# Performance work log

Hardware: AMD Instinct MI355X
Metric: run time of the kernel (lower is better)

## Reference

```python
import jax, jax.numpy as jnp
import numpy as np

TEMPERATURE = 0.5
EPSILON = 1e-9


def _l2_normalize(x, eps=1e-12):
    # matches torch F.normalize(p=2, dim=-1): x / max(||x||, eps)
    n = jnp.linalg.norm(x, axis=-1, keepdims=True)
    return x / jnp.maximum(n, eps)


def setup_inputs() -> dict:
    key = jax.random.key(0)
    k1, k2, k3 = jax.random.split(key, 3)
    N, D, V = 8192, 128, 3
    H_consensus = jax.random.normal(k1, (N, D), dtype=jnp.float32)
    S_similarity = jax.random.uniform(k2, (N, N), dtype=jnp.float32)
    H_views = jax.random.normal(k3, (V, N, D), dtype=jnp.float32)
    return {"H_consensus": H_consensus, "S_similarity": S_similarity, "H_views": H_views}


def reference(H_consensus, S_similarity, H_views):
    N = H_consensus.shape[0]
    V = H_views.shape[0]
    Hc = _l2_normalize(H_consensus)            # [N, D]
    Hv = _l2_normalize(H_views)                # [V, N, D]
    sim = jnp.einsum('nd,vmd->vnm', Hc, Hv)    # [V, N, N]
    positive = jnp.diagonal(sim, axis1=1, axis2=2) / TEMPERATURE  # [V, N]
    weights = 1.0 - S_similarity               # [N, N], broadcast over V
    denom = jnp.sum(weights * jnp.exp(sim / TEMPERATURE), axis=-1)  # [V, N]
    denom = jnp.maximum(denom, EPSILON)
    loss = -(positive - jnp.log(denom))        # [V, N]
    return jnp.sum(loss) / (N * V)
```

## Files before the change

### kernel.cpp

```cpp
#include <hip/hip_runtime.h>
#include <hip/hip_bf16.h>

constexpr int kN = 8192;
constexpr int kD = 128;
constexpr int kV = 3;
constexpr int kNV = kV * kN;
constexpr int kNChunk = 512;
constexpr int kNTile = 32;
constexpr int kIters = kNChunk / kNTile;
constexpr int kAccStride = 529;

typedef __attribute__((ext_vector_type(8))) short bf16x8;
typedef __attribute__((ext_vector_type(4))) float floatx4;

__device__ __forceinline__ unsigned pack_bf16(float a, float b) {
    unsigned ua = __float_as_uint(a);
    unsigned ub = __float_as_uint(b);
    ua = (ua + 0x7FFFu + ((ua >> 16) & 1u)) >> 16;
    ub = (ub + 0x7FFFu + ((ub >> 16) & 1u)) >> 16;
    return ua | (ub << 16);
}

__global__ void k_normalize(const float* __restrict__ Hc, const float* __restrict__ Hv,
                            unsigned* __restrict__ HcB, unsigned* __restrict__ HvB) {
    int row  = (blockIdx.x * blockDim.x + threadIdx.x) >> 6;
    int lane = threadIdx.x & 63;
    const float* src;
    unsigned* dst;
    float extra;
    if (row < kN) { src = Hc + (size_t)row * kD; dst = HcB + (size_t)row * (kD / 2); extra = 2.0f; }
    else {
        int r = row - kN;
        src = Hv + (size_t)r * kD; dst = HvB + (size_t)r * (kD / 2); extra = 1.0f;
    }
    float2 x = ((const float2*)src)[lane];
    float ss = x.x * x.x + x.y * x.y;
    ss += __shfl_xor(ss, 1);  ss += __shfl_xor(ss, 2);  ss += __shfl_xor(ss, 4);
    ss += __shfl_xor(ss, 8);  ss += __shfl_xor(ss, 16); ss += __shfl_xor(ss, 32);
    float inv = extra * rsqrtf(fmaxf(ss, 1e-24f));
    dst[lane] = pack_bf16(x.x * inv, x.y * inv);
}

__global__ void k_positive(const unsigned* __restrict__ HcB, const unsigned* __restrict__ HvB,
                           float* __restrict__ pos_partial) {
    int row  = (blockIdx.x * blockDim.x + threadIdx.x) >> 6;
    int lane = threadIdx.x & 63;
    int w    = threadIdx.x >> 6;
    int n    = row & (kN - 1);
    unsigned a = HcB[(size_t)n * (kD / 2) + lane];
    unsigned b = HvB[(size_t)row * (kD / 2) + lane];
    float dot = __uint_as_float(a << 16) * __uint_as_float(b << 16)
              + __uint_as_float(a & 0xFFFF0000u) * __uint_as_float(b & 0xFFFF0000u);
    dot += __shfl_xor(dot, 1);  dot += __shfl_xor(dot, 2);  dot += __shfl_xor(dot, 4);
    dot += __shfl_xor(dot, 8);  dot += __shfl_xor(dot, 16); dot += __shfl_xor(dot, 32);
    __shared__ float acc4[4];
    if (lane == 0) acc4[w] = dot;
    __syncthreads();
    if (threadIdx.x == 0)
        atomicAdd(&pos_partial[blockIdx.x & 255], acc4[0] + acc4[1] + acc4[2] + acc4[3]);
}

__launch_bounds__(256, 3)
__global__ void k_main(const unsigned* __restrict__ HcB, const unsigned* __restrict__ HvB,
                       const float* __restrict__ S, float* __restrict__ denom) {
    __shared__ float Stile[2][kNTile * 68];
    __shared__ short Htile[2][kNTile * 136];
    __shared__ float accum[kV * kAccStride];

    const int tid  = threadIdx.x;
    const int w    = tid >> 6;
    const int lane = tid & 63;
    const int col  = lane & 15;
    const int quad = lane >> 4;
    const int m0b  = blockIdx.x * 64;
    const int m0w  = m0b + w * 16;
    const int nbase = blockIdx.y * kNChunk;
    const int sr = tid >> 4;
    const int sc = tid & 15;

    for (int i = tid; i < kV * kAccStride; i += 256) accum[i] = 0.f;

    bf16x8 afrag[kV][4];
#pragma unroll
    for (int v = 0; v < kV; ++v) {
        const short* rowp = (const short*)HvB + ((size_t)(v * kN + m0w + col)) * kD;
#pragma unroll
        for (int kk = 0; kk < 4; ++kk)
            afrag[v][kk] = *(const bf16x8*)(rowp + kk * 32 + quad * 8);
    }

    const short* hc = (const short*)HcB;

    {
        int n0 = nbase;
        float4 sa = *(const float4*)(S + (size_t)(n0 + sr) * kN + m0b + sc * 4);
        float4 sb = *(const float4*)(S + (size_t)(n0 + sr + 16) * kN + m0b + sc * 4);
        float4 ha = *(const float4*)(hc + (size_t)(n0 + sr) * kD + sc * 8);
        float4 hb = *(const float4*)(hc + (size_t)(n0 + sr + 16) * kD + sc * 8);
        *(float4*)&Stile[0][sr * 68 + sc * 4]        = sa;
        *(float4*)&Stile[0][(sr + 16) * 68 + sc * 4] = sb;
        *(float4*)&Htile[0][sr * 136 + sc * 8]        = ha;
        *(float4*)&Htile[0][(sr + 16) * 136 + sc * 8] = hb;
    }
    __syncthreads();

    for (int it = 0; it < kIters; ++it) {
        int itn = (it + 1 < kIters) ? it + 1 : it;
        int n0n = nbase + itn * kNTile;
        float4 sa = *(const float4*)(S + (size_t)(n0n + sr) * kN + m0b + sc * 4);
        float4 sb = *(const float4*)(S + (size_t)(n0n + sr + 16) * kN + m0b + sc * 4);
        float4 ha = *(const float4*)(hc + (size_t)(n0n + sr) * kD + sc * 8);
        float4 hb = *(const float4*)(hc + (size_t)(n0n + sr + 16) * kD + sc * 8);

        const int cur = it & 1;
#pragma unroll
        for (int sub = 0; sub < 2; ++sub) {
            const int nrow = sub * 16 + col;
            bf16x8 bfrag[4];
#pragma unroll
            for (int kk = 0; kk < 4; ++kk)
                bfrag[kk] = *(const bf16x8*)&Htile[cur][nrow * 136 + kk * 32 + quad * 8];
            float4 s4 = *(const float4*)&Stile[cur][nrow * 68 + w * 16 + quad * 4];

            floatx4 acc0 = {0.f,0.f,0.f,0.f}, acc1 = {0.f,0.f,0.f,0.f}, acc2 = {0.f,0.f,0.f,0.f};
#pragma unroll
            for (int kk = 0; kk < 4; ++kk) {
                acc0 = __builtin_amdgcn_mfma_f32_16x16x32_bf16(afrag[0][kk], bfrag[kk], acc0, 0, 0, 0);
                acc1 = __builtin_amdgcn_mfma_f32_16x16x32_bf16(afrag[1][kk], bfrag[kk], acc1, 0, 0, 0);
                acc2 = __builtin_amdgcn_mfma_f32_16x16x32_bf16(afrag[2][kk], bfrag[kk], acc2, 0, 0, 0);
            }
            float w0 = 1.f - s4.x, w1 = 1.f - s4.y, w2 = 1.f - s4.z, w3 = 1.f - s4.w;
            float p0 = w0 * __expf(acc0[0]) + w1 * __expf(acc0[1]) + w2 * __expf(acc0[2]) + w3 * __expf(acc0[3]);
            float p1 = w0 * __expf(acc1[0]) + w1 * __expf(acc1[1]) + w2 * __expf(acc1[2]) + w3 * __expf(acc1[3]);
            float p2 = w0 * __expf(acc2[0]) + w1 * __expf(acc2[1]) + w2 * __expf(acc2[2]) + w3 * __expf(acc2[3]);
            p0 += __shfl_xor(p0, 16); p0 += __shfl_xor(p0, 32);
            p1 += __shfl_xor(p1, 16); p1 += __shfl_xor(p1, 32);
            p2 += __shfl_xor(p2, 16); p2 += __shfl_xor(p2, 32);
            float val = (quad == 0) ? p0 : ((quad == 1) ? p1 : p2);
            if (quad < 3)
                atomicAdd(&accum[quad * kAccStride + it * kNTile + sub * 16 + col], val);
        }

        const int nxt = cur ^ 1;
        *(float4*)&Stile[nxt][sr * 68 + sc * 4]        = sa;
        *(float4*)&Stile[nxt][(sr + 16) * 68 + sc * 4] = sb;
        *(float4*)&Htile[nxt][sr * 136 + sc * 8]        = ha;
        *(float4*)&Htile[nxt][(sr + 16) * 136 + sc * 8] = hb;
        __syncthreads();
    }

    for (int i = tid; i < kV * kNChunk; i += 256) {
        int v = i >> 9, c = i & (kNChunk - 1);
        atomicAdd(&denom[(size_t)v * kN + nbase + c], accum[v * kAccStride + c]);
    }
}

__global__ void k_final(const float* __restrict__ denom, const float* __restrict__ pos_partial,
                        float* __restrict__ out) {
    int idx  = blockIdx.x * 256 + threadIdx.x;
    int lane = threadIdx.x & 63;
    int w    = threadIdx.x >> 6;
    float val = logf(fmaxf(denom[idx], 1e-9f));
    if (blockIdx.x == 0) val -= pos_partial[threadIdx.x];
    val += __shfl_xor(val, 1);  val += __shfl_xor(val, 2);  val += __shfl_xor(val, 4);
    val += __shfl_xor(val, 8);  val += __shfl_xor(val, 16); val += __shfl_xor(val, 32);
    __shared__ float acc4[4];
    if (lane == 0) acc4[w] = val;
    __syncthreads();
    if (threadIdx.x == 0)
        atomicAdd(out, (acc4[0] + acc4[1] + acc4[2] + acc4[3]) * (1.0f / kNV));
}

extern "C" void kernel_launch(void* const* d_in, const int* in_sizes, int n_in,
                              void* d_out, int out_size, void* d_ws, size_t ws_size,
                              hipStream_t stream) {
    const float* Hc = (const float*)d_in[0];
    const float* S  = (const float*)d_in[1];
    const float* Hv = (const float*)d_in[2];

    unsigned* HcB  = (unsigned*)d_ws;
    unsigned* HvB  = HcB + (size_t)kN * (kD / 2);
    float*    den  = (float*)(HvB + (size_t)kV * kN * (kD / 2));
    float*    posp = den + kNV;
    float*    outF = (float*)d_out;

    hipMemsetAsync(den, 0, ((size_t)kNV + 256) * sizeof(float), stream);
    hipMemsetAsync(outF, 0, sizeof(float), stream);

    k_normalize<<<dim3((kN + kV * kN) / 4), 256, 0, stream>>>(Hc, Hv, HcB, HvB);
    k_positive<<<dim3(kNV / 4), 256, 0, stream>>>(HcB, HvB, posp);
    k_main<<<dim3(kN / 64, kN / kNChunk), dim3(256), 0, stream>>>(HcB, HvB, S, den);
    k_final<<<dim3(kNV / 256), dim3(256), 0, stream>>>(den, posp, outF);
}
```

Measured before the change: 431.3 us.

## Load S directly into registers, use exp2 with prescaled Hc, permlane quad reductions

Removes the shared-memory staging of the S tile: each lane now loads its own S values straight from global memory into registers and prefetches the next iteration's values. The Hc normalization scale is folded to 2/ln2 so the hardware exp2 can replace __expf, and the positive term is multiplied by ln2 in the final kernel to compensate. The cross-quad shuffles are replaced with v_permlane16/32_swap inline asm. Per-lane S loads are less coalesced than the old tiled loads, and the inline asm depends on the target supporting these permlane instructions.

```diff
diff --git a/kernel.cpp b/kernel.cpp
--- a/kernel.cpp
+++ b/kernel.cpp
@@ -9,9 +9,17 @@
 constexpr int kNTile = 32;
 constexpr int kIters = kNChunk / kNTile;
 constexpr int kAccStride = 529;
+constexpr float kLn2 = 0.6931471805599453f;
+constexpr float kScaleHc = 2.885390081777927f;
 
 typedef __attribute__((ext_vector_type(8))) short bf16x8;
 typedef __attribute__((ext_vector_type(4))) float floatx4;
+
+#if __has_builtin(__builtin_amdgcn_exp2f)
+#define EXP2F(x) __builtin_amdgcn_exp2f(x)
+#else
+#define EXP2F(x) exp2f(x)
+#endif
 
 __device__ __forceinline__ unsigned pack_bf16(float a, float b) {
     unsigned ua = __float_as_uint(a);
@@ -19,6 +27,15 @@
     ua = (ua + 0x7FFFu + ((ua >> 16) & 1u)) >> 16;
     ub = (ub + 0x7FFFu + ((ub >> 16) & 1u)) >> 16;
     return ua | (ub << 16);
+}
+
+__device__ __forceinline__ float quad_sum(float p) {
+    float t = p;
+    asm("v_permlane16_swap_b32 %0, %1" : "+v"(p), "+v"(t));
+    p += t;
+    t = p;
+    asm("v_permlane32_swap_b32 %0, %1" : "+v"(p), "+v"(t));
+    return p + t;
 }
 
 __global__ void k_normalize(const float* __restrict__ Hc, const float* __restrict__ Hv,
@@ -28,7 +45,7 @@
     const float* src;
     unsigned* dst;
     float extra;
-    if (row < kN) { src = Hc + (size_t)row * kD; dst = HcB + (size_t)row * (kD / 2); extra = 2.0f; }
+    if (row < kN) { src = Hc + (size_t)row * kD; dst = HcB + (size_t)row * (kD / 2); extra = kScaleHc; }
     else {
         int r = row - kN;
         src = Hv + (size_t)r * kD; dst = HvB + (size_t)r * (kD / 2); extra = 1.0f;
@@ -63,7 +80,6 @@
 __launch_bounds__(256, 3)
 __global__ void k_main(const unsigned* __restrict__ HcB, const unsigned* __restrict__ HvB,
                        const float* __restrict__ S, float* __restrict__ denom) {
-    __shared__ float Stile[2][kNTile * 68];
     __shared__ short Htile[2][kNTile * 136];
     __shared__ float accum[kV * kAccStride];
 
@@ -90,27 +106,25 @@
     }
 
     const short* hc = (const short*)HcB;
+    const float* Sp = S + (size_t)(nbase + col) * kN + m0b + (w << 4) + (quad << 2);
 
     {
-        int n0 = nbase;
-        float4 sa = *(const float4*)(S + (size_t)(n0 + sr) * kN + m0b + sc * 4);
-        float4 sb = *(const float4*)(S + (size_t)(n0 + sr + 16) * kN + m0b + sc * 4);
-        float4 ha = *(const float4*)(hc + (size_t)(n0 + sr) * kD + sc * 8);
-        float4 hb = *(const float4*)(hc + (size_t)(n0 + sr + 16) * kD + sc * 8);
-        *(float4*)&Stile[0][sr * 68 + sc * 4]        = sa;
-        *(float4*)&Stile[0][(sr + 16) * 68 + sc * 4] = sb;
+        float4 ha = *(const float4*)(hc + (size_t)(nbase + sr) * kD + sc * 8);
+        float4 hb = *(const float4*)(hc + (size_t)(nbase + sr + 16) * kD + sc * 8);
         *(float4*)&Htile[0][sr * 136 + sc * 8]        = ha;
         *(float4*)&Htile[0][(sr + 16) * 136 + sc * 8] = hb;
     }
+    float4 s0 = *(const float4*)(Sp);
+    float4 s1 = *(const float4*)(Sp + (size_t)16 * kN);
     __syncthreads();
 
     for (int it = 0; it < kIters; ++it) {
         int itn = (it + 1 < kIters) ? it + 1 : it;
         int n0n = nbase + itn * kNTile;
-        float4 sa = *(const float4*)(S + (size_t)(n0n + sr) * kN + m0b + sc * 4);
-        float4 sb = *(const float4*)(S + (size_t)(n0n + sr + 16) * kN + m0b + sc * 4);
-        float4 ha = *(const float4*)(hc + (size_t)(n0n + sr) * kD + sc * 8);
-        float4 hb = *(const float4*)(hc + (size_t)(n0n + sr + 16) * kD + sc * 8);
+        float4 ha  = *(const float4*)(hc + (size_t)(n0n + sr) * kD + sc * 8);
+        float4 hb  = *(const float4*)(hc + (size_t)(n0n + sr + 16) * kD + sc * 8);
+        float4 s0n = *(const float4*)(Sp + (size_t)(itn * 32) * kN);
+        float4 s1n = *(const float4*)(Sp + (size_t)(itn * 32 + 16) * kN);
 
         const int cur = it & 1;
 #pragma unroll
@@ -120,7 +134,7 @@
 #pragma unroll
             for (int kk = 0; kk < 4; ++kk)
                 bfrag[kk] = *(const bf16x8*)&Htile[cur][nrow * 136 + kk * 32 + quad * 8];
-            float4 s4 = *(const float4*)&Stile[cur][nrow * 68 + w * 16 + quad * 4];
+            float4 s4 = sub ? s1 : s0;
 
             floatx4 acc0 = {0.f,0.f,0.f,0.f}, acc1 = {0.f,0.f,0.f,0.f}, acc2 = {0.f,0.f,0.f,0.f};
 #pragma unroll
@@ -130,20 +144,19 @@
                 acc2 = __builtin_amdgcn_mfma_f32_16x16x32_bf16(afrag[2][kk], bfrag[kk], acc2, 0, 0, 0);
             }
             float w0 = 1.f - s4.x, w1 = 1.f - s4.y, w2 = 1.f - s4.z, w3 = 1.f - s4.w;
-            float p0 = w0 * __expf(acc0[0]) + w1 * __expf(acc0[1]) + w2 * __expf(acc0[2]) + w3 * __expf(acc0[3]);
-            float p1 = w0 * __expf(acc1[0]) + w1 * __expf(acc1[1]) + w2 * __expf(acc1[2]) + w3 * __expf(acc1[3]);
-            float p2 = w0 * __expf(acc2[0]) + w1 * __expf(acc2[1]) + w2 * __expf(acc2[2]) + w3 * __expf(acc2[3]);
-            p0 += __shfl_xor(p0, 16); p0 += __shfl_xor(p0, 32);
-            p1 += __shfl_xor(p1, 16); p1 += __shfl_xor(p1, 32);
-            p2 += __shfl_xor(p2, 16); p2 += __shfl_xor(p2, 32);
+            float p0 = w0 * EXP2F(acc0[0]) + w1 * EXP2F(acc0[1]) + w2 * EXP2F(acc0[2]) + w3 * EXP2F(acc0[3]);
+            float p1 = w0 * EXP2F(acc1[0]) + w1 * EXP2F(acc1[1]) + w2 * EXP2F(acc1[2]) + w3 * EXP2F(acc1[3]);
+            float p2 = w0 * EXP2F(acc2[0]) + w1 * EXP2F(acc2[1]) + w2 * EXP2F(acc2[2]) + w3 * EXP2F(acc2[3]);
+            p0 = quad_sum(p0);
+            p1 = quad_sum(p1);
+            p2 = quad_sum(p2);
             float val = (quad == 0) ? p0 : ((quad == 1) ? p1 : p2);
             if (quad < 3)
                 atomicAdd(&accum[quad * kAccStride + it * kNTile + sub * 16 + col], val);
         }
 
+        s0 = s0n; s1 = s1n;
         const int nxt = cur ^ 1;
-        *(float4*)&Stile[nxt][sr * 68 + sc * 4]        = sa;
-        *(float4*)&Stile[nxt][(sr + 16) * 68 + sc * 4] = sb;
         *(float4*)&Htile[nxt][sr * 136 + sc * 8]        = ha;
         *(float4*)&Htile[nxt][(sr + 16) * 136 + sc * 8] = hb;
         __syncthreads();
@@ -161,7 +174,7 @@
     int lane = threadIdx.x & 63;
     int w    = threadIdx.x >> 6;
     float val = logf(fmaxf(denom[idx], 1e-9f));
-    if (blockIdx.x == 0) val -= pos_partial[threadIdx.x];
+    if (blockIdx.x == 0) val -= pos_partial[threadIdx.x] * kLn2;
     val += __shfl_xor(val, 1);  val += __shfl_xor(val, 2);  val += __shfl_xor(val, 4);
     val += __shfl_xor(val, 8);  val += __shfl_xor(val, 16); val += __shfl_xor(val, 32);
     __shared__ float acc4[4];
```

Result: faster. 412.7 us (-4.3%).
